# Kernel tuning notes

Hardware: AMD Instinct MI355X
Metric: run time of the kernel (lower is better)

Reference implementation:

```python
import jax, jax.numpy as jnp
import numpy as np

B = 16            # num sequences (decode: 1 query token each)
MAX_BLOCKS = 256  # blocks per sequence
BLOCK_SIZE = 16
NUM_BLOCKS = B * MAX_BLOCKS
HQ, HKV, HD = 32, 8, 128
SCALE = HD ** -0.5
NEG = -1e30


def setup_inputs() -> dict:
    key = jax.random.key(0)
    ks = jax.random.split(key, 6)
    q = jax.random.normal(ks[0], (B, HQ, HD), jnp.float32)
    k = jax.random.normal(ks[1], (B, HKV, HD), jnp.float32)
    v = jax.random.normal(ks[2], (B, HKV, HD), jnp.float32)
    k_cache = jax.random.normal(ks[3], (NUM_BLOCKS, BLOCK_SIZE, HKV, HD), jnp.float32)
    v_cache = jax.random.normal(ks[4], (NUM_BLOCKS, BLOCK_SIZE, HKV, HD), jnp.float32)
    # each sequence owns a disjoint contiguous set of blocks
    block_tables = jnp.arange(B * MAX_BLOCKS, dtype=jnp.int64).reshape(B, MAX_BLOCKS)
    seq_lens = jax.random.randint(ks[5], (B,), 2048, MAX_BLOCKS * BLOCK_SIZE + 1).astype(jnp.int64)
    last = seq_lens - 1  # slot of the token being written this step
    slot_mapping = block_tables[jnp.arange(B), last // BLOCK_SIZE] * BLOCK_SIZE + last % BLOCK_SIZE
    query_lens = jnp.ones((B,), jnp.int64)
    return {"q": q, "k": k, "v": v, "k_cache": k_cache, "v_cache": v_cache,
            "slot_mapping": slot_mapping, "block_tables": block_tables,
            "seq_lens": seq_lens, "query_lens": query_lens, "is_prefill": False}


def reference(q, k, v, k_cache, v_cache, slot_mapping, block_tables, seq_lens, query_lens, is_prefill):
    nb, bs, hkv, hd = k_cache.shape
    # write_kv_cache: scatter new k/v tokens into flat slot view of the caches
    kc = k_cache.reshape(nb * bs, hkv, hd).at[slot_mapping].set(k).reshape(nb, bs, hkv, hd)
    vc = v_cache.reshape(nb * bs, hkv, hd).at[slot_mapping].set(v).reshape(nb, bs, hkv, hd)
    b = q.shape[0]
    # gather blocks per sequence: (B, max_blocks, bs, hkv, hd) -> (B, kv_len, hkv, hd)
    K = kc[block_tables].reshape(b, -1, hkv, hd)
    V = vc[block_tables].reshape(b, -1, hkv, hd)
    kv_len = K.shape[1]
    valid = jnp.arange(kv_len)[None, :] < seq_lens[:, None]  # (B, kv_len)
    g = q.shape[1] // hkv  # GQA groups; q head k*g+j attends with kv head k
    qg = q.reshape(b, hkv, g, hd)
    scores = jnp.einsum('bkgd,bskd->bkgs', qg, K) * SCALE  # (B, hkv, g, kv_len)
    scores = jnp.where(valid[:, None, None, :], scores, NEG)
    p = jax.nn.softmax(scores, axis=-1)
    out = jnp.einsum('bkgs,bskd->bkgd', p, V).reshape(b, hkv * g, hd)
    return out
```

## Files before the change

kernel.cpp:

```cpp
#include <hip/hip_runtime.h>

#define NBATCH 16
#define MAXB 256
#define BS 16
#define HQ 32
#define HKV 8
#define G 4
#define HD 128
#define SCALE 0.08838834764831845f
#define NEGF -1.0e30f
#define NEGI -2.0e30f
#define RESCALE_THR 8.0f

__device__ __forceinline__ float dot8(const float4 a0, const float4 a1,
                                      const float4 b0, const float4 b1) {
  return a0.x*b0.x + a0.y*b0.y + a0.z*b0.z + a0.w*b0.w +
         a1.x*b1.x + a1.y*b1.y + a1.z*b1.z + a1.w*b1.w;
}

template<int CTL>
__device__ __forceinline__ float dpp_row_add(float v) {
  const int s = __builtin_amdgcn_update_dpp(0, __float_as_int(v), CTL, 0xF, 0xF, true);
  return v + __int_as_float(s);
}
__device__ __forceinline__ float row_reduce_add(float v) {
  v = dpp_row_add<0x128>(v);
  v = dpp_row_add<0x124>(v);
  v = dpp_row_add<0x122>(v);
  v = dpp_row_add<0x121>(v);
  return v;
}

__global__ __launch_bounds__(256) void pa_split(
    const float* __restrict__ q,
    const float* __restrict__ knew,
    const float* __restrict__ vnew,
    const float* __restrict__ k_cache,
    const float* __restrict__ v_cache,
    const int* __restrict__ block_tables,
    const int* __restrict__ seq_lens,
    float* __restrict__ part_ml,
    float* __restrict__ part_acc,
    int nsplit)
{
  const int hg    = blockIdx.x & 1;
  const int b     = (blockIdx.x >> 1) % NBATCH;
  const int split = blockIdx.x / (2 * NBATCH);
  const int h     = hg * 4 + (threadIdx.x >> 6);
  const int lane  = threadIdx.x & 63;
  const int tg    = lane >> 4;
  const int tl    = lane & 15;

  const int seq_len = seq_lens[b];
  int per = (seq_len + nsplit - 1) / nsplit;
  per = (per + 15) & ~15;
  const int s0 = split * per;
  const int s1 = min(seq_len, s0 + per);
  const int last = seq_len - 1;
  const size_t pidx = (size_t)(b*HKV + h)*nsplit + split;

  if (s0 >= seq_len) {
    if (tg == 0) {
      if (tl == 0) {
#pragma unroll
        for (int j = 0; j < G; ++j) {
          part_ml[(pidx*G + j)*2 + 0] = NEGF;
          part_ml[(pidx*G + j)*2 + 1] = 0.f;
        }
      }
      const float4 z = make_float4(0.f,0.f,0.f,0.f);
#pragma unroll
      for (int j = 0; j < G; ++j) {
        float4* ap = (float4*)(part_acc + (pidx*G + j)*HD + tl*8);
        ap[0] = z; ap[1] = z;
      }
    }
    return;
  }

  float4 q0[G], q1[G];
#pragma unroll
  for (int j = 0; j < G; ++j) {
    const float* qp = q + (size_t)(b*HQ + h*G + j)*HD + tl*8;
    q0[j] = ((const float4*)qp)[0];
    q1[j] = ((const float4*)qp)[1];
  }

  float m[G], l[G];
  float4 a0[G], a1[G];
#pragma unroll
  for (int j = 0; j < G; ++j) {
    m[j] = NEGF; l[j] = 0.f;
    a0[j] = make_float4(0.f,0.f,0.f,0.f);
    a1[j] = make_float4(0.f,0.f,0.f,0.f);
  }

  const float* knp = knew + (size_t)(b*HKV + h)*HD + tl*8;
  const float* vnp = vnew + (size_t)(b*HKV + h)*HD + tl*8;
  const int btbase = b * MAXB;

  auto loadG = [&](float4 (&kr)[2], float4 (&vr)[2], const int blk, const int pos) {
    const int s = pos + tg;
    const size_t off = ((size_t)blk*BS + (s & 15))*(HKV*HD) + (size_t)h*HD + tl*8;
    const float* kp = k_cache + off;
    const float* vp = v_cache + off;
    if (s == last) { kp = knp; vp = vnp; }
    kr[0] = ((const float4*)kp)[0];
    kr[1] = ((const float4*)kp)[1];
    vr[0] = ((const float4*)vp)[0];
    vr[1] = ((const float4*)vp)[1];
  };

  auto computeG = [&](const float4 (&kr)[2], const float4 (&vr)[2], const int pos) {
    const bool valid = (pos + tg) < s1;
    float sc[G];
#pragma unroll
    for (int j = 0; j < G; ++j) {
      float p = dot8(q0[j], q1[j], kr[0], kr[1]);
      p = row_reduce_add(p);
      sc[j] = valid ? p * SCALE : NEGI;
    }
    bool need = false;
#pragma unroll
    for (int j = 0; j < G; ++j) need = need || (sc[j] > m[j] + RESCALE_THR);
    if (__any(need)) {
#pragma unroll
      for (int j = 0; j < G; ++j) {
        const float mn = fmaxf(m[j], sc[j]);
        const float f  = __expf(m[j] - mn);
        l[j] *= f;
        a0[j].x *= f; a0[j].y *= f; a0[j].z *= f; a0[j].w *= f;
        a1[j].x *= f; a1[j].y *= f; a1[j].z *= f; a1[j].w *= f;
        m[j] = mn;
      }
    }
#pragma unroll
    for (int j = 0; j < G; ++j) {
      const float pp = __expf(sc[j] - m[j]);
      l[j] += pp;
      a0[j].x += pp*vr[0].x; a0[j].y += pp*vr[0].y;
      a0[j].z += pp*vr[0].z; a0[j].w += pp*vr[0].w;
      a1[j].x += pp*vr[1].x; a1[j].y += pp*vr[1].y;
      a1[j].z += pp*vr[1].z; a1[j].w += pp*vr[1].w;
    }
  };

  const int npos   = s1 - s0;
  const int npages = (npos + 15) >> 4;
  const int pg0    = s0 >> 4;

  float4 kA[2], vA[2], kB[2], vB[2], kC[2], vC[2], kD[2], vD[2];

  int blkCur  = block_tables[btbase + pg0];
  int blkNext = block_tables[btbase + pg0 + ((npages > 1) ? 1 : 0)];

  loadG(kA, vA, blkCur, s0);
  loadG(kB, vB, blkCur, s0 + 4);
  loadG(kC, vC, blkCur, s0 + 8);
  loadG(kD, vD, blkCur, s0 + 12);

  for (int p = 0; p < npages; ++p) {
    const int base  = s0 + p*16;
    const bool more = (p + 1 < npages);
    const int blkL  = blkNext;
    const int lbase = base + 16;
    const int pnn   = (p + 2 < npages) ? (p + 2) : (npages - 1);
    const int blkNN = block_tables[btbase + pg0 + pnn];

    computeG(kA, vA, base);
    if (more) loadG(kA, vA, blkL, lbase);
    computeG(kB, vB, base + 4);
    if (more) loadG(kB, vB, blkL, lbase + 4);
    computeG(kC, vC, base + 8);
    if (more) loadG(kC, vC, blkL, lbase + 8);
    computeG(kD, vD, base + 12);
    if (more) loadG(kD, vD, blkL, lbase + 12);

    blkNext = blkNN;
  }

#pragma unroll
  for (int mask = 16; mask <= 32; mask <<= 1) {
#pragma unroll
    for (int j = 0; j < G; ++j) {
      const float mo = __shfl_xor(m[j], mask, 64);
      const float lo = __shfl_xor(l[j], mask, 64);
      const float mn = fmaxf(m[j], mo);
      const float f0 = __expf(m[j] - mn);
      const float f1 = __expf(mo  - mn);
      l[j] = l[j]*f0 + lo*f1;
      float t;
      t = __shfl_xor(a0[j].x, mask, 64); a0[j].x = a0[j].x*f0 + t*f1;
      t = __shfl_xor(a0[j].y, mask, 64); a0[j].y = a0[j].y*f0 + t*f1;
      t = __shfl_xor(a0[j].z, mask, 64); a0[j].z = a0[j].z*f0 + t*f1;
      t = __shfl_xor(a0[j].w, mask, 64); a0[j].w = a0[j].w*f0 + t*f1;
      t = __shfl_xor(a1[j].x, mask, 64); a1[j].x = a1[j].x*f0 + t*f1;
      t = __shfl_xor(a1[j].y, mask, 64); a1[j].y = a1[j].y*f0 + t*f1;
      t = __shfl_xor(a1[j].z, mask, 64); a1[j].z = a1[j].z*f0 + t*f1;
      t = __shfl_xor(a1[j].w, mask, 64); a1[j].w = a1[j].w*f0 + t*f1;
      m[j] = mn;
    }
  }

  if (tg == 0) {
    if (tl == 0) {
#pragma unroll
      for (int j = 0; j < G; ++j) {
        part_ml[(pidx*G + j)*2 + 0] = m[j];
        part_ml[(pidx*G + j)*2 + 1] = l[j];
      }
    }
#pragma unroll
    for (int j = 0; j < G; ++j) {
      float4* ap = (float4*)(part_acc + (pidx*G + j)*HD + tl*8);
      ap[0] = a0[j];
      ap[1] = a1[j];
    }
  }
}

__global__ __launch_bounds__(128) void pa_reduce(
    const float* __restrict__ part_ml,
    const float* __restrict__ part_acc,
    float* __restrict__ out,
    int P)
{
  const int qh = blockIdx.x % HQ;
  const int b  = blockIdx.x / HQ;
  const int h  = qh >> 2;
  const int j  = qh & 3;
  const int d  = threadIdx.x;

  const size_t base = (size_t)(b*HKV + h) * P;
  float mg = NEGF;
  for (int p = 0; p < P; ++p)
    mg = fmaxf(mg, part_ml[((base + p)*G + j)*2 + 0]);

  float lsum = 0.f, asum = 0.f;
  for (int p = 0; p < P; ++p) {
    const float mm = part_ml[((base + p)*G + j)*2 + 0];
    const float ll = part_ml[((base + p)*G + j)*2 + 1];
    const float f  = __expf(mm - mg);
    lsum += f * ll;
    asum += f * part_acc[((base + p)*G + j)*HD + d];
  }
  out[(size_t)(b*HQ + qh)*HD + d] = asum / lsum;
}

extern "C" void kernel_launch(void* const* d_in, const int* in_sizes, int n_in,
                              void* d_out, int out_size, void* d_ws, size_t ws_size,
                              hipStream_t stream) {
  const float* q  = (const float*)d_in[0];
  const float* k  = (const float*)d_in[1];
  const float* v  = (const float*)d_in[2];
  const float* kc = (const float*)d_in[3];
  const float* vc = (const float*)d_in[4];
  const int* bt = (const int*)d_in[6];
  const int* sl = (const int*)d_in[7];

  int nsplit = 32;
  for (;;) {
    const size_t need = (size_t)NBATCH * HKV * nsplit * G * (2 + HD) * sizeof(float);
    if (need <= ws_size || nsplit == 1) break;
    nsplit >>= 1;
  }
  float* part_ml  = (float*)d_ws;
  float* part_acc = part_ml + (size_t)NBATCH * HKV * nsplit * G * 2;

  hipLaunchKernelGGL(pa_split, dim3(NBATCH * nsplit * 2), dim3(256), 0, stream,
                     q, k, v, kc, vc, bt, sl, part_ml, part_acc, nsplit);
  hipLaunchKernelGGL(pa_reduce, dim3(NBATCH * HQ), dim3(128), 0, stream,
                     part_ml, part_acc, (float*)d_out, nsplit);
}
```

Before: 105.5 us.

## Raise split count, use interleaved float4 lane mapping, drop software prefetch

Changes the per-lane head-dim mapping so each 16-lane group reads two contiguous 256-byte halves instead of each lane reading 32 contiguous bytes, aiming for better coalesced loads. Removes the register double-buffered prefetch of the next page in favour of load-then-compute per page. Raises the default split count from 32 to 128, quadrupling the number of workgroups for more memory-level parallelism, at the cost of a larger reduction pass and more partial-result traffic.

```diff
diff --git a/kernel.cpp b/kernel.cpp
--- a/kernel.cpp
+++ b/kernel.cpp
@@ -71,8 +71,8 @@
       const float4 z = make_float4(0.f,0.f,0.f,0.f);
 #pragma unroll
       for (int j = 0; j < G; ++j) {
-        float4* ap = (float4*)(part_acc + (pidx*G + j)*HD + tl*8);
-        ap[0] = z; ap[1] = z;
+        *(float4*)(part_acc + (pidx*G + j)*HD + tl*4)      = z;
+        *(float4*)(part_acc + (pidx*G + j)*HD + 64 + tl*4) = z;
       }
     }
     return;
@@ -81,9 +81,9 @@
   float4 q0[G], q1[G];
 #pragma unroll
   for (int j = 0; j < G; ++j) {
-    const float* qp = q + (size_t)(b*HQ + h*G + j)*HD + tl*8;
-    q0[j] = ((const float4*)qp)[0];
-    q1[j] = ((const float4*)qp)[1];
+    const float* qp = q + (size_t)(b*HQ + h*G + j)*HD;
+    q0[j] = *(const float4*)(qp + tl*4);
+    q1[j] = *(const float4*)(qp + 64 + tl*4);
   }
 
   float m[G], l[G];
@@ -95,20 +95,19 @@
     a1[j] = make_float4(0.f,0.f,0.f,0.f);
   }
 
-  const float* knp = knew + (size_t)(b*HKV + h)*HD + tl*8;
-  const float* vnp = vnew + (size_t)(b*HKV + h)*HD + tl*8;
+  const float* knp = knew + (size_t)(b*HKV + h)*HD;
+  const float* vnp = vnew + (size_t)(b*HKV + h)*HD;
   const int btbase = b * MAXB;
 
   auto loadG = [&](float4 (&kr)[2], float4 (&vr)[2], const int blk, const int pos) {
     const int s = pos + tg;
-    const size_t off = ((size_t)blk*BS + (s & 15))*(HKV*HD) + (size_t)h*HD + tl*8;
-    const float* kp = k_cache + off;
-    const float* vp = v_cache + off;
+    const float* kp = k_cache + ((size_t)blk*BS + (s & 15))*(HKV*HD) + (size_t)h*HD;
+    const float* vp = v_cache + ((size_t)blk*BS + (s & 15))*(HKV*HD) + (size_t)h*HD;
     if (s == last) { kp = knp; vp = vnp; }
-    kr[0] = ((const float4*)kp)[0];
-    kr[1] = ((const float4*)kp)[1];
-    vr[0] = ((const float4*)vp)[0];
-    vr[1] = ((const float4*)vp)[1];
+    kr[0] = *(const float4*)(kp + tl*4);
+    kr[1] = *(const float4*)(kp + 64 + tl*4);
+    vr[0] = *(const float4*)(vp + tl*4);
+    vr[1] = *(const float4*)(vp + 64 + tl*4);
   };
 
   auto computeG = [&](const float4 (&kr)[2], const float4 (&vr)[2], const int pos) {
@@ -145,38 +144,19 @@
     }
   };
 
-  const int npos   = s1 - s0;
-  const int npages = (npos + 15) >> 4;
-  const int pg0    = s0 >> 4;
-
   float4 kA[2], vA[2], kB[2], vB[2], kC[2], vC[2], kD[2], vD[2];
-
-  int blkCur  = block_tables[btbase + pg0];
-  int blkNext = block_tables[btbase + pg0 + ((npages > 1) ? 1 : 0)];
-
-  loadG(kA, vA, blkCur, s0);
-  loadG(kB, vB, blkCur, s0 + 4);
-  loadG(kC, vC, blkCur, s0 + 8);
-  loadG(kD, vD, blkCur, s0 + 12);
-
-  for (int p = 0; p < npages; ++p) {
-    const int base  = s0 + p*16;
-    const bool more = (p + 1 < npages);
-    const int blkL  = blkNext;
-    const int lbase = base + 16;
-    const int pnn   = (p + 2 < npages) ? (p + 2) : (npages - 1);
-    const int blkNN = block_tables[btbase + pg0 + pnn];
-
+  int blk = block_tables[btbase + (s0 >> 4)];
+  for (int base = s0; base < s1; base += 16) {
+    const int nblk = (base + 16 < s1) ? block_tables[btbase + (base >> 4) + 1] : blk;
+    loadG(kA, vA, blk, base);
+    loadG(kB, vB, blk, base + 4);
+    loadG(kC, vC, blk, base + 8);
+    loadG(kD, vD, blk, base + 12);
     computeG(kA, vA, base);
-    if (more) loadG(kA, vA, blkL, lbase);
     computeG(kB, vB, base + 4);
-    if (more) loadG(kB, vB, blkL, lbase + 4);
     computeG(kC, vC, base + 8);
-    if (more) loadG(kC, vC, blkL, lbase + 8);
     computeG(kD, vD, base + 12);
-    if (more) loadG(kD, vD, blkL, lbase + 12);
-
-    blkNext = blkNN;
+    blk = nblk;
   }
 
 #pragma unroll
@@ -212,9 +192,8 @@
     }
 #pragma unroll
     for (int j = 0; j < G; ++j) {
-      float4* ap = (float4*)(part_acc + (pidx*G + j)*HD + tl*8);
-      ap[0] = a0[j];
-      ap[1] = a1[j];
+      *(float4*)(part_acc + (pidx*G + j)*HD + tl*4)      = a0[j];
+      *(float4*)(part_acc + (pidx*G + j)*HD + 64 + tl*4) = a1[j];
     }
   }
 }
@@ -258,7 +237,7 @@
   const int* bt = (const int*)d_in[6];
   const int* sl = (const int*)d_in[7];
 
-  int nsplit = 32;
+  int nsplit = 128;
   for (;;) {
     const size_t need = (size_t)NBATCH * HKV * nsplit * G * (2 + HD) * sizeof(float);
     if (need <= ws_size || nsplit == 1) break;
```

Result: slower. 151.9 us (+44.0%).

## Fuse split-KV reduction into attention kernel via last-block atomic counter

Applied to the files above, without the earlier changes.

Drops the separate reduce kernel. Each split block now bumps an atomic counter per (batch, head-group), and the last block to finish merges all partial softmax states and writes the output with vectorized float4 loads. The per-thread dimension mapping also changes from 8 contiguous floats to two 4-float chunks 64 apart, and the split count becomes a compile-time constant. This saves one kernel launch and its tail, at the cost of a memset launch, thread fences and a serialized reduction inside the last block. The early exit for empty splits is removed, but seq_len >= 2048 means every split has work here.

```diff
diff --git a/kernel.cpp b/kernel.cpp
--- a/kernel.cpp
+++ b/kernel.cpp
@@ -11,6 +11,7 @@
 #define NEGF -1.0e30f
 #define NEGI -2.0e30f
 #define RESCALE_THR 8.0f
+#define NSPLIT 32
 
 __device__ __forceinline__ float dot8(const float4 a0, const float4 a1,
                                       const float4 b0, const float4 b1) {
@@ -39,9 +40,10 @@
     const float* __restrict__ v_cache,
     const int* __restrict__ block_tables,
     const int* __restrict__ seq_lens,
+    int*   __restrict__ cnt,
     float* __restrict__ part_ml,
     float* __restrict__ part_acc,
-    int nsplit)
+    float* __restrict__ out)
 {
   const int hg    = blockIdx.x & 1;
   const int b     = (blockIdx.x >> 1) % NBATCH;
@@ -52,38 +54,19 @@
   const int tl    = lane & 15;
 
   const int seq_len = seq_lens[b];
-  int per = (seq_len + nsplit - 1) / nsplit;
+  int per = (seq_len + NSPLIT - 1) / NSPLIT;
   per = (per + 15) & ~15;
   const int s0 = split * per;
   const int s1 = min(seq_len, s0 + per);
   const int last = seq_len - 1;
-  const size_t pidx = (size_t)(b*HKV + h)*nsplit + split;
-
-  if (s0 >= seq_len) {
-    if (tg == 0) {
-      if (tl == 0) {
-#pragma unroll
-        for (int j = 0; j < G; ++j) {
-          part_ml[(pidx*G + j)*2 + 0] = NEGF;
-          part_ml[(pidx*G + j)*2 + 1] = 0.f;
-        }
-      }
-      const float4 z = make_float4(0.f,0.f,0.f,0.f);
-#pragma unroll
-      for (int j = 0; j < G; ++j) {
-        float4* ap = (float4*)(part_acc + (pidx*G + j)*HD + tl*8);
-        ap[0] = z; ap[1] = z;
-      }
-    }
-    return;
-  }
+  const size_t pidx = (size_t)(b*HKV + h)*NSPLIT + split;
 
   float4 q0[G], q1[G];
 #pragma unroll
   for (int j = 0; j < G; ++j) {
-    const float* qp = q + (size_t)(b*HQ + h*G + j)*HD + tl*8;
-    q0[j] = ((const float4*)qp)[0];
-    q1[j] = ((const float4*)qp)[1];
+    const float* qp = q + (size_t)(b*HQ + h*G + j)*HD;
+    q0[j] = *(const float4*)(qp + tl*4);
+    q1[j] = *(const float4*)(qp + 64 + tl*4);
   }
 
   float m[G], l[G];
@@ -95,20 +78,19 @@
     a1[j] = make_float4(0.f,0.f,0.f,0.f);
   }
 
-  const float* knp = knew + (size_t)(b*HKV + h)*HD + tl*8;
-  const float* vnp = vnew + (size_t)(b*HKV + h)*HD + tl*8;
+  const float* knp = knew + (size_t)(b*HKV + h)*HD;
+  const float* vnp = vnew + (size_t)(b*HKV + h)*HD;
   const int btbase = b * MAXB;
 
   auto loadG = [&](float4 (&kr)[2], float4 (&vr)[2], const int blk, const int pos) {
     const int s = pos + tg;
-    const size_t off = ((size_t)blk*BS + (s & 15))*(HKV*HD) + (size_t)h*HD + tl*8;
-    const float* kp = k_cache + off;
-    const float* vp = v_cache + off;
+    const float* kp = k_cache + ((size_t)blk*BS + (s & 15))*(HKV*HD) + (size_t)h*HD;
+    const float* vp = v_cache + ((size_t)blk*BS + (s & 15))*(HKV*HD) + (size_t)h*HD;
     if (s == last) { kp = knp; vp = vnp; }
-    kr[0] = ((const float4*)kp)[0];
-    kr[1] = ((const float4*)kp)[1];
-    vr[0] = ((const float4*)vp)[0];
-    vr[1] = ((const float4*)vp)[1];
+    kr[0] = *(const float4*)(kp + tl*4);
+    kr[1] = *(const float4*)(kp + 64 + tl*4);
+    vr[0] = *(const float4*)(vp + tl*4);
+    vr[1] = *(const float4*)(vp + 64 + tl*4);
   };
 
   auto computeG = [&](const float4 (&kr)[2], const float4 (&vr)[2], const int pos) {
@@ -145,38 +127,40 @@
     }
   };
 
-  const int npos   = s1 - s0;
-  const int npages = (npos + 15) >> 4;
-  const int pg0    = s0 >> 4;
-
-  float4 kA[2], vA[2], kB[2], vB[2], kC[2], vC[2], kD[2], vD[2];
-
-  int blkCur  = block_tables[btbase + pg0];
-  int blkNext = block_tables[btbase + pg0 + ((npages > 1) ? 1 : 0)];
-
-  loadG(kA, vA, blkCur, s0);
-  loadG(kB, vB, blkCur, s0 + 4);
-  loadG(kC, vC, blkCur, s0 + 8);
-  loadG(kD, vD, blkCur, s0 + 12);
-
-  for (int p = 0; p < npages; ++p) {
-    const int base  = s0 + p*16;
-    const bool more = (p + 1 < npages);
-    const int blkL  = blkNext;
-    const int lbase = base + 16;
-    const int pnn   = (p + 2 < npages) ? (p + 2) : (npages - 1);
-    const int blkNN = block_tables[btbase + pg0 + pnn];
-
-    computeG(kA, vA, base);
-    if (more) loadG(kA, vA, blkL, lbase);
-    computeG(kB, vB, base + 4);
-    if (more) loadG(kB, vB, blkL, lbase + 4);
-    computeG(kC, vC, base + 8);
-    if (more) loadG(kC, vC, blkL, lbase + 8);
-    computeG(kD, vD, base + 12);
-    if (more) loadG(kD, vD, blkL, lbase + 12);
-
-    blkNext = blkNN;
+  {
+    const int npos   = s1 - s0;
+    const int npages = (npos + 15) >> 4;
+    const int pg0    = s0 >> 4;
+
+    float4 kA[2], vA[2], kB[2], vB[2], kC[2], vC[2], kD[2], vD[2];
+
+    int blkCur  = block_tables[btbase + pg0];
+    int blkNext = block_tables[btbase + pg0 + ((npages > 1) ? 1 : 0)];
+
+    loadG(kA, vA, blkCur, s0);
+    loadG(kB, vB, blkCur, s0 + 4);
+    loadG(kC, vC, blkCur, s0 + 8);
+    loadG(kD, vD, blkCur, s0 + 12);
+
+    for (int p = 0; p < npages; ++p) {
+      const int base  = s0 + p*16;
+      const bool more = (p + 1 < npages);
+      const int blkL  = blkNext;
+      const int lbase = base + 16;
+      const int pnn   = (p + 2 < npages) ? (p + 2) : (npages - 1);
+      const int blkNN = block_tables[btbase + pg0 + pnn];
+
+      computeG(kA, vA, base);
+      if (more) loadG(kA, vA, blkL, lbase);
+      computeG(kB, vB, base + 4);
+      if (more) loadG(kB, vB, blkL, lbase + 4);
+      computeG(kC, vC, base + 8);
+      if (more) loadG(kC, vC, blkL, lbase + 8);
+      computeG(kD, vD, base + 12);
+      if (more) loadG(kD, vD, blkL, lbase + 12);
+
+      blkNext = blkNN;
+    }
   }
 
 #pragma unroll
@@ -212,39 +196,49 @@
     }
 #pragma unroll
     for (int j = 0; j < G; ++j) {
-      float4* ap = (float4*)(part_acc + (pidx*G + j)*HD + tl*8);
-      ap[0] = a0[j];
-      ap[1] = a1[j];
-    }
-  }
-}
-
-__global__ __launch_bounds__(128) void pa_reduce(
-    const float* __restrict__ part_ml,
-    const float* __restrict__ part_acc,
-    float* __restrict__ out,
-    int P)
-{
-  const int qh = blockIdx.x % HQ;
-  const int b  = blockIdx.x / HQ;
-  const int h  = qh >> 2;
-  const int j  = qh & 3;
-  const int d  = threadIdx.x;
-
-  const size_t base = (size_t)(b*HKV + h) * P;
+      *(float4*)(part_acc + (pidx*G + j)*HD + tl*4)      = a0[j];
+      *(float4*)(part_acc + (pidx*G + j)*HD + 64 + tl*4) = a1[j];
+    }
+  }
+
+  __threadfence();
+  __syncthreads();
+  __shared__ int is_last;
+  if (threadIdx.x == 0)
+    is_last = (atomicAdd(&cnt[b*2 + hg], 1) == NSPLIT*1 - 1) ? 1 : 0;
+  __syncthreads();
+  if (!is_last) return;
+  __threadfence();
+
+  const int qi = threadIdx.x >> 4;
+  const int t2 = threadIdx.x & 15;
+  const int hh = hg*4 + (qi >> 2);
+  const int jj = qi & 3;
+  const size_t rbase = (size_t)(b*HKV + hh)*NSPLIT;
+  const int d0 = t2*8;
+
   float mg = NEGF;
-  for (int p = 0; p < P; ++p)
-    mg = fmaxf(mg, part_ml[((base + p)*G + j)*2 + 0]);
-
-  float lsum = 0.f, asum = 0.f;
-  for (int p = 0; p < P; ++p) {
-    const float mm = part_ml[((base + p)*G + j)*2 + 0];
-    const float ll = part_ml[((base + p)*G + j)*2 + 1];
+  for (int p = 0; p < NSPLIT; ++p)
+    mg = fmaxf(mg, part_ml[((rbase + p)*G + jj)*2 + 0]);
+
+  float ls = 0.f;
+  float4 s0v = make_float4(0.f,0.f,0.f,0.f);
+  float4 s1v = make_float4(0.f,0.f,0.f,0.f);
+  for (int p = 0; p < NSPLIT; ++p) {
+    const float mm = part_ml[((rbase + p)*G + jj)*2 + 0];
+    const float ll = part_ml[((rbase + p)*G + jj)*2 + 1];
     const float f  = __expf(mm - mg);
-    lsum += f * ll;
-    asum += f * part_acc[((base + p)*G + j)*HD + d];
-  }
-  out[(size_t)(b*HQ + qh)*HD + d] = asum / lsum;
+    ls += f * ll;
+    const float* ap = part_acc + ((rbase + p)*G + jj)*HD + d0;
+    const float4 x0 = *(const float4*)(ap);
+    const float4 x1 = *(const float4*)(ap + 4);
+    s0v.x += f*x0.x; s0v.y += f*x0.y; s0v.z += f*x0.z; s0v.w += f*x0.w;
+    s1v.x += f*x1.x; s1v.y += f*x1.y; s1v.z += f*x1.z; s1v.w += f*x1.w;
+  }
+  const float inv = 1.f / ls;
+  float* op = out + (size_t)(b*HQ + hh*G + jj)*HD + d0;
+  *(float4*)(op)     = make_float4(s0v.x*inv, s0v.y*inv, s0v.z*inv, s0v.w*inv);
+  *(float4*)(op + 4) = make_float4(s1v.x*inv, s1v.y*inv, s1v.z*inv, s1v.w*inv);
 }
 
 extern "C" void kernel_launch(void* const* d_in, const int* in_sizes, int n_in,
@@ -258,17 +252,12 @@
   const int* bt = (const int*)d_in[6];
   const int* sl = (const int*)d_in[7];
 
-  int nsplit = 32;
-  for (;;) {
-    const size_t need = (size_t)NBATCH * HKV * nsplit * G * (2 + HD) * sizeof(float);
-    if (need <= ws_size || nsplit == 1) break;
-    nsplit >>= 1;
-  }
-  float* part_ml  = (float*)d_ws;
-  float* part_acc = part_ml + (size_t)NBATCH * HKV * nsplit * G * 2;
-
-  hipLaunchKernelGGL(pa_split, dim3(NBATCH * nsplit * 2), dim3(256), 0, stream,
-                     q, k, v, kc, vc, bt, sl, part_ml, part_acc, nsplit);
-  hipLaunchKernelGGL(pa_reduce, dim3(NBATCH * HQ), dim3(128), 0, stream,
-                     part_ml, part_acc, (float*)d_out, nsplit);
-}
+  int*   cnt      = (int*)d_ws;
+  float* part_ml  = (float*)((char*)d_ws + 256);
+  float* part_acc = part_ml + (size_t)NBATCH * HKV * NSPLIT * G * 2;
+
+  hipMemsetAsync(cnt, 0, NBATCH * 2 * sizeof(int), stream);
+
+  hipLaunchKernelGGL(pa_split, dim3(NBATCH * NSPLIT * 2), dim3(256), 0, stream,
+                     q, k, v, kc, vc, bt, sl, cnt, part_ml, part_acc, (float*)d_out);
+}
```

Result: slower. 296.7 us (+181.3%).
